# Performance work log

Hardware: AMD Instinct MI355X
Metric: run time of the kernel (lower is better)

Reference implementation:

```python
import jax, jax.numpy as jnp
import numpy as np

B, L, D, K, MAXL = 2, 1024, 256, 64, 1024
EPS = 1e-5

def _encode(x, pos, w1, b1, w2, b2, wa, ba):
    # x: [B,L,D] -> complex phasors [B,L,K]
    xa = x + pos[: x.shape[1]][None]
    h = jax.nn.gelu(xa @ w1 + b1, approximate=False)
    phase = jnp.tanh(h @ w2 + b2) * np.float32(np.pi)
    amp = jax.nn.softplus(xa @ wa + ba) + np.float32(0.1)
    return (amp * jnp.exp(1j * phase)).astype(jnp.complex64)

def setup_inputs() -> dict:
    key = jax.random.key(0)
    ks = jax.random.split(key, 24)
    def lin_w(k, i, o):
        return (jax.random.normal(k, (i, o), jnp.float32) / np.sqrt(np.float32(i)))
    def pos(k):
        return jax.random.normal(k, (MAXL, D), jnp.float32) * np.float32(0.02)
    inp = {
        'x': jax.random.normal(ks[0], (B, L, D), jnp.float32),
        'pos_k': pos(ks[1]),
        'w1_k': lin_w(ks[2], D, D), 'b1_k': jnp.zeros((D,), jnp.float32),
        'w2_k': lin_w(ks[3], D, K), 'b2_k': jnp.zeros((K,), jnp.float32),
        'wa_k': lin_w(ks[4], D, K), 'ba_k': jnp.zeros((K,), jnp.float32),
        'pos_q': pos(ks[5]),
        'w1_q': lin_w(ks[6], D, D), 'b1_q': jnp.zeros((D,), jnp.float32),
        'w2_q': lin_w(ks[7], D, K), 'b2_q': jnp.zeros((K,), jnp.float32),
        'wa_q': lin_w(ks[8], D, K), 'ba_q': jnp.zeros((K,), jnp.float32),
        'wv': lin_w(ks[9], D, D), 'bv': jnp.zeros((D,), jnp.float32),
        'ln_g': jnp.ones((D,), jnp.float32), 'ln_b': jnp.zeros((D,), jnp.float32),
        'wo': lin_w(ks[10], D, D), 'bo': jnp.zeros((D,), jnp.float32),
    }
    return inp

def reference(x, pos_k, w1_k, b1_k, w2_k, b2_k, wa_k, ba_k,
              pos_q, w1_q, b1_q, w2_q, b2_q, wa_q, ba_q,
              wv, bv, ln_g, ln_b, wo, bo):
    Bx, Lx, Dx = x.shape
    kp = _encode(x, pos_k, w1_k, b1_k, w2_k, b2_k, wa_k, ba_k)  # [B,L,K] complex
    qp = _encode(x, pos_q, w1_q, b1_q, w2_q, b2_q, wa_q, ba_q)  # [B,L,K] complex
    V = (x @ wv + bv).astype(jnp.complex64)                      # [B,L,D]
    bound = kp[:, :, :, None] * V[:, :, None, :]                 # [B,L,K,D]
    memory = jnp.cumsum(bound, axis=1)                           # [B,L,K,D]
    retrieved = jnp.real(jnp.einsum('blkd,blk->bld', memory, jnp.conj(qp)))
    positions = jnp.arange(1, Lx + 1, dtype=jnp.float32)
    norm = jnp.sqrt(positions * np.float32(kp.shape[-1]))[None, :, None]
    r = retrieved / norm
    mu = jnp.mean(r, axis=-1, keepdims=True)
    var = jnp.var(r, axis=-1, keepdims=True)
    rn = (r - mu) / jnp.sqrt(var + np.float32(EPS)) * ln_g + ln_b
    return x + rn @ wo + bo
```

## Files before the change

kernel.cpp:

```cpp
#include <hip/hip_runtime.h>
#include <hip/hip_bf16.h>

typedef __attribute__((ext_vector_type(8))) short short8;
typedef __attribute__((ext_vector_type(4))) float float4v;

constexpr int B = 2, L = 1024, D = 256, K = 64;
constexpr int N = B * L;
constexpr int NC = L / 64;

constexpr int WT2_OFF = 524288;

__device__ __forceinline__ ushort bf16_hi(float v) {
  return (ushort)(__float_as_uint(v) >> 16);
}
__device__ __forceinline__ float hi_f(float v) {
  return __uint_as_float(__float_as_uint(v) & 0xFFFF0000u);
}
__device__ __forceinline__ ushort bf16_rne(float v) {
  uint b = __float_as_uint(v);
  b += 0x7FFF + ((b >> 16) & 1);
  return (ushort)(b >> 16);
}

__global__ __launch_bounds__(256) void prep_kernel(
    const float* __restrict__ w1_k, const float* __restrict__ w1_q,
    const float* __restrict__ wv, const float* __restrict__ wo,
    const float* __restrict__ w2_k, const float* __restrict__ wa_k,
    const float* __restrict__ w2_q, const float* __restrict__ wa_q,
    ushort* __restrict__ WT) {
  __shared__ float Lt[64][65];
  const int bi = blockIdx.x, tid = threadIdx.x;
  const float* src;
  int ncols, k0, n0;
  ushort* dhi;
  int losz;
  if (bi < 64) {
    const int m = bi >> 4, t = bi & 15;
    src = (m == 0) ? w1_k : (m == 1) ? w1_q : (m == 2) ? wv : wo;
    ncols = 256; k0 = (t >> 2) * 64; n0 = (t & 3) * 64;
    dhi = WT + m * 131072; losz = 65536;
  } else {
    const int m = (bi - 64) >> 2, kt = (bi - 64) & 3;
    src = (m == 0) ? w2_k : (m == 1) ? wa_k : (m == 2) ? w2_q : wa_q;
    ncols = 64; k0 = kt * 64; n0 = 0;
    dhi = WT + WT2_OFF + m * 32768; losz = 16384;
  }
  ushort* dlo = dhi + losz;
  for (int p = 0; p < 16; ++p) {
    const int kr = p * 4 + (tid >> 6), nc = tid & 63;
    Lt[kr][nc] = src[(k0 + kr) * ncols + n0 + nc];
  }
  __syncthreads();
  const int n = tid >> 2, kq = tid & 3;
  uint uh[8], ul[8];
  for (int i = 0; i < 8; ++i) {
    const float v0 = Lt[kq * 16 + 2 * i][n];
    const float v1 = Lt[kq * 16 + 2 * i + 1][n];
    uh[i] = (uint)bf16_hi(v0) | ((uint)bf16_hi(v1) << 16);
    ul[i] = (uint)bf16_rne(v0 - hi_f(v0)) | ((uint)bf16_rne(v1 - hi_f(v1)) << 16);
  }
  const int oidx = (n0 + n) * 256 + k0 + kq * 16;
  *(uint4*)&dhi[oidx] = make_uint4(uh[0], uh[1], uh[2], uh[3]);
  *(uint4*)&dhi[oidx + 8] = make_uint4(uh[4], uh[5], uh[6], uh[7]);
  *(uint4*)&dlo[oidx] = make_uint4(ul[0], ul[1], ul[2], ul[3]);
  *(uint4*)&dlo[oidx + 8] = make_uint4(ul[4], ul[5], ul[6], ul[7]);
}

__global__ __launch_bounds__(256) void enc1_kernel(
    const float* __restrict__ x, const float* __restrict__ pos_k,
    const float* __restrict__ pos_q,
    const float* __restrict__ b1_k, const float* __restrict__ b1_q,
    const float* __restrict__ bv, const ushort* __restrict__ WT,
    float* __restrict__ hk, float* __restrict__ hq, float* __restrict__ V) {
  __shared__ __align__(16) ushort Ah[32][40], Al[32][40];
  __shared__ __align__(16) ushort Bh[128][40], Bl[128][40];
  const int tid = threadIdx.x;
  const int g = blockIdx.x / 128;
  const int rem = blockIdx.x % 128;
  const int row0 = (rem >> 1) * 32, nb = (rem & 1) * 128;
  const float* pos = (g == 0) ? pos_k : (g == 1) ? pos_q : nullptr;
  const ushort* Wh = WT + g * 131072;
  const ushort* Wl = Wh + 65536;
  const int w = tid >> 6, lane = tid & 63;
  const int m16 = lane & 15, quad = lane >> 4;

  float4v acc[2][2] = {};

  for (int k0 = 0; k0 < 256; k0 += 32) {
    __syncthreads();
    {
      const int r = tid >> 3, kc = (tid & 7) * 4;
      const int row = row0 + r, l = row & (L - 1);
      float4 xv = *(const float4*)&x[row * D + k0 + kc];
      if (pos) {
        const float4 pv = *(const float4*)&pos[l * D + k0 + kc];
        xv.x += pv.x; xv.y += pv.y; xv.z += pv.z; xv.w += pv.w;
      }
      ushort4 h4, l4;
      h4.x = bf16_hi(xv.x); l4.x = bf16_rne(xv.x - hi_f(xv.x));
      h4.y = bf16_hi(xv.y); l4.y = bf16_rne(xv.y - hi_f(xv.y));
      h4.z = bf16_hi(xv.z); l4.z = bf16_rne(xv.z - hi_f(xv.z));
      h4.w = bf16_hi(xv.w); l4.w = bf16_rne(xv.w - hi_f(xv.w));
      *(ushort4*)&Ah[r][kc] = h4;
      *(ushort4*)&Al[r][kc] = l4;
    }
#pragma unroll
    for (int p = 0; p < 2; ++p) {
      const int n = (tid >> 2) + p * 64, chunk = tid & 3;
      const int ga = (nb + n) * 256 + k0 + chunk * 8;
      *(uint4*)&Bh[n][chunk * 8] = *(const uint4*)&Wh[ga];
      *(uint4*)&Bl[n][chunk * 8] = *(const uint4*)&Wl[ga];
    }
    __syncthreads();

    short8 afh[2], afl[2], bfh[2], bfl[2];
#pragma unroll
    for (int r = 0; r < 2; ++r) {
      afh[r] = *(const short8*)&Ah[r * 16 + m16][quad * 8];
      afl[r] = *(const short8*)&Al[r * 16 + m16][quad * 8];
    }
#pragma unroll
    for (int c = 0; c < 2; ++c) {
      const int col = w * 32 + c * 16 + m16;
      bfh[c] = *(const short8*)&Bh[col][quad * 8];
      bfl[c] = *(const short8*)&Bl[col][quad * 8];
    }
#pragma unroll
    for (int r = 0; r < 2; ++r)
#pragma unroll
      for (int c = 0; c < 2; ++c) {
        acc[r][c] = __builtin_amdgcn_mfma_f32_16x16x32_bf16(afh[r], bfh[c], acc[r][c], 0, 0, 0);
        acc[r][c] = __builtin_amdgcn_mfma_f32_16x16x32_bf16(afh[r], bfl[c], acc[r][c], 0, 0, 0);
        acc[r][c] = __builtin_amdgcn_mfma_f32_16x16x32_bf16(afl[r], bfh[c], acc[r][c], 0, 0, 0);
      }
  }

  float* outp = (g == 0) ? hk : (g == 1) ? hq : V;
  const float* bp = (g == 0) ? b1_k : (g == 1) ? b1_q : bv;
#pragma unroll
  for (int c = 0; c < 2; ++c) {
    const int colg = nb + w * 32 + c * 16 + m16;
    const float bias = bp[colg];
#pragma unroll
    for (int r = 0; r < 2; ++r)
#pragma unroll
      for (int j = 0; j < 4; ++j) {
        const int rowg = row0 + r * 16 + quad * 4 + j;
        float v = acc[r][c][j] + bias;
        if (g < 2) v = 0.5f * v * (1.0f + erff(v * 0.70710678f));
        outp[rowg * D + colg] = v;
      }
  }
}

__global__ __launch_bounds__(512) void enc2_kernel(
    const float* __restrict__ x, const float* __restrict__ pos_k,
    const float* __restrict__ pos_q, const float* __restrict__ hk,
    const float* __restrict__ hq,
    const float* __restrict__ b2_k, const float* __restrict__ ba_k,
    const float* __restrict__ b2_q, const float* __restrict__ ba_q,
    const ushort* __restrict__ WT,
    float* __restrict__ kr, float* __restrict__ ki,
    float* __restrict__ qr, float* __restrict__ qi) {
  __shared__ __align__(16) ushort Ahh[16][40], Ahl[16][40], Axh[16][40], Axl[16][40];
  __shared__ __align__(16) ushort B2h[64][40], B2l[64][40], Bah[64][40], Bal[64][40];
  __shared__ float phL[16][68], amL[16][68];
  const int tid = threadIdx.x;
  const int e = blockIdx.x >> 7;
  const int r0g = (blockIdx.x & 127) * 16;
  const float* hsrc = e ? hq : hk;
  const float* pos = e ? pos_q : pos_k;
  const ushort* W2h = WT + WT2_OFF + (e ? 2 : 0) * 32768;
  const ushort* W2l = W2h + 16384;
  const ushort* Wah = WT + WT2_OFF + (e ? 3 : 1) * 32768;
  const ushort* Wal = Wah + 16384;
  const int w = tid >> 6, lane = tid & 63;
  const int m16 = lane & 15, quad = lane >> 4;
  const int mat = w & 1, ct = w >> 1;

  float4v acc = {};
  for (int k0 = 0; k0 < 256; k0 += 32) {
    __syncthreads();
    {
      const int half = tid >> 8;
      const int t2 = tid & 255;
      const int r = t2 >> 4, kc = (t2 & 15) * 2;
      const int row = r0g + r, l = row & (L - 1);
      if (half == 0) {
        const float2 hv = *(const float2*)&hsrc[row * D + k0 + kc];
        ushort2 h2, l2;
        h2.x = bf16_hi(hv.x); l2.x = bf16_rne(hv.x - hi_f(hv.x));
        h2.y = bf16_hi(hv.y); l2.y = bf16_rne(hv.y - hi_f(hv.y));
        *(ushort2*)&Ahh[r][kc] = h2;
        *(ushort2*)&Ahl[r][kc] = l2;
      } else {
        const float2 xv = *(const float2*)&x[row * D + k0 + kc];
        const float2 pv = *(const float2*)&pos[l * D + k0 + kc];
        const float a0 = xv.x + pv.x, a1 = xv.y + pv.y;
        ushort2 h2, l2;
        h2.x = bf16_hi(a0); l2.x = bf16_rne(a0 - hi_f(a0));
        h2.y = bf16_hi(a1); l2.y = bf16_rne(a1 - hi_f(a1));
        *(ushort2*)&Axh[r][kc] = h2;
        *(ushort2*)&Axl[r][kc] = l2;
      }
    }
    {
      const int sel = tid >> 7;
      const int idx = tid & 127;
      const int n = idx >> 1, ch = (idx & 1) * 2;
      const int ga = n * 256 + k0 + ch * 8;
      const ushort* s = (sel == 0) ? W2h : (sel == 1) ? W2l : (sel == 2) ? Wah : Wal;
      ushort* dst = (sel == 0) ? &B2h[n][ch * 8] : (sel == 1) ? &B2l[n][ch * 8]
                  : (sel == 2) ? &Bah[n][ch * 8] : &Bal[n][ch * 8];
      *(uint4*)dst = *(const uint4*)&s[ga];
      *(uint4*)(dst + 8) = *(const uint4*)&s[ga + 8];
    }
    __syncthreads();

    const short8 ah = mat ? *(const short8*)&Axh[m16][quad * 8]
                          : *(const short8*)&Ahh[m16][quad * 8];
    const short8 al = mat ? *(const short8*)&Axl[m16][quad * 8]
                          : *(const short8*)&Ahl[m16][quad * 8];
    const int col = ct * 16 + m16;
    const short8 bh = mat ? *(const short8*)&Bah[col][quad * 8]
                          : *(const short8*)&B2h[col][quad * 8];
    const short8 bl = mat ? *(const short8*)&Bal[col][quad * 8]
                          : *(const short8*)&B2l[col][quad * 8];
    acc = __builtin_amdgcn_mfma_f32_16x16x32_bf16(ah, bh, acc, 0, 0, 0);
    acc = __builtin_amdgcn_mfma_f32_16x16x32_bf16(ah, bl, acc, 0, 0, 0);
    acc = __builtin_amdgcn_mfma_f32_16x16x32_bf16(al, bh, acc, 0, 0, 0);
  }

  {
    const int colk = ct * 16 + m16;
    if (mat == 0) {
      const float b2v = (e ? b2_q : b2_k)[colk];
#pragma unroll
      for (int j = 0; j < 4; ++j)
        phL[quad * 4 + j][colk] = tanhf(acc[j] + b2v) * 3.14159265358979f;
    } else {
      const float bav = (e ? ba_q : ba_k)[colk];
#pragma unroll
      for (int j = 0; j < 4; ++j) {
        const float av = acc[j] + bav;
        amL[quad * 4 + j][colk] = fmaxf(av, 0.0f) + log1pf(expf(-fabsf(av))) + 0.1f;
      }
    }
  }
  __syncthreads();
  {
    float* pr = e ? qr : kr;
    float* pim = e ? qi : ki;
#pragma unroll
    for (int p = 0; p < 2; ++p) {
      const int idx = p * 512 + tid;
      const int r = idx >> 6, ccol = idx & 63;
      const int row = r0g + r;
      const float a = amL[r][ccol], pph = phL[r][ccol];
      pr[row * K + ccol] = a * cosf(pph);
      pim[row * K + ccol] = a * sinf(pph);
    }
  }
}

__global__ __launch_bounds__(256) void tbuild_kernel(
    const float* __restrict__ kr, const float* __restrict__ ki,
    const float* __restrict__ V, float* __restrict__ TMt) {
  const int id = blockIdx.x;
  const int dc = id & 15, c = (id >> 4) & 15, b = id >> 8;
  const int tid = threadIdx.x;
  const int n0 = b * L + c * 64;
  const int dl = tid & 15;
  const int kb = tid >> 4;

  __shared__ float krL[64][68], kiL[64][68];
  __shared__ float VL[64][20];
  __shared__ float Tl[16][204];
  for (int e = tid; e < 1024; e += 256) {
    const int t = e >> 4, k4 = (e & 15) * 4;
    *(float4*)&krL[t][k4] = *(const float4*)&kr[(n0 + t) * K + k4];
    *(float4*)&kiL[t][k4] = *(const float4*)&ki[(n0 + t) * K + k4];
  }
  {
    const int t = tid >> 2, f = (tid & 3) * 4;
    *(float4*)&VL[t][f] = *(const float4*)&V[(n0 + t) * D + dc * 16 + f];
  }
  __syncthreads();

  {
    const int t0 = (tid >> 4) * 4;
#pragma unroll
    for (int i = 0; i < 4; ++i) Tl[dl][128 + t0 + i] = VL[t0 + i][dl];
  }

  float ar[4] = {0.f, 0.f, 0.f, 0.f}, ai[4] = {0.f, 0.f, 0.f, 0.f};
#pragma unroll 4
  for (int t = 0; t < 64; ++t) {
    const float vt = VL[t][dl];
    const float4 k4r = *(const float4*)&krL[t][kb * 4];
    const float4 k4i = *(const float4*)&kiL[t][kb * 4];
    ar[0] += k4r.x * vt; ar[1] += k4r.y * vt; ar[2] += k4r.z * vt; ar[3] += k4r.w * vt;
    ai[0] += k4i.x * vt; ai[1] += k4i.y * vt; ai[2] += k4i.z * vt; ai[3] += k4i.w * vt;
  }

#pragma unroll
  for (int i = 0; i < 4; ++i) {
    Tl[dl][kb * 4 + i] = ar[i];
    Tl[dl][64 + kb * 4 + i] = ai[i];
  }
  __syncthreads();

  float* dst = &TMt[(((size_t)(b * 16 + c)) * 256 + dc * 16) * 192];
#pragma unroll
  for (int p = 0; p < 3; ++p) {
    const int e = p * 256 + tid;
    const int row = e / 48, f4 = e % 48;
    *(float4*)&dst[(size_t)row * 192 + f4 * 4] = *(const float4*)&Tl[row][f4 * 4];
  }
}

__global__ __launch_bounds__(512) void ret_kernel(
    const float* __restrict__ qr, const float* __restrict__ qi,
    const float* __restrict__ kr, const float* __restrict__ ki,
    const float* __restrict__ TMt, float* __restrict__ ret,
    float* __restrict__ LNred) {
  __shared__ __align__(16) ushort Ah[64][200], Al[64][200];
  __shared__ __align__(16) ushort Kh[64][136], Kl[64][136];
  __shared__ __align__(16) ushort Bh[32][200], Bl[32][200];
  const int tid = threadIdx.x;
  const int dc = blockIdx.x & 7;
  const int c = (blockIdx.x >> 3) & 15;
  const int b = blockIdx.x >> 7;
  const int n0 = b * L + c * 64;
  const int cols0 = dc * 32;
  const int w = tid >> 6, lane = tid & 63;
  const int m16 = lane & 15, quad = lane >> 4;

#pragma unroll
  for (int j = 0; j < 4; ++j) {
    const int e = j * 512 + tid;
    const int row = e >> 5, c4 = e & 31;
    const int col0 = (c4 & 15) * 4;
    const int acol = (c4 < 16 ? 0 : 64) + col0;
    {
      const float* src = (c4 < 16) ? qr : qi;
      const float4 v = *(const float4*)&src[(n0 + row) * K + col0];
      ushort4 h4, l4;
      h4.x = bf16_hi(v.x); l4.x = bf16_rne(v.x - hi_f(v.x));
      h4.y = bf16_hi(v.y); l4.y = bf16_rne(v.y - hi_f(v.y));
      h4.z = bf16_hi(v.z); l4.z = bf16_rne(v.z - hi_f(v.z));
      h4.w = bf16_hi(v.w); l4.w = bf16_rne(v.w - hi_f(v.w));
      *(ushort4*)&Ah[row][acol] = h4;
      *(ushort4*)&Al[row][acol] = l4;
    }
    {
      const float* src = (c4 < 16) ? kr : ki;
      const float4 v = *(const float4*)&src[(n0 + row) * K + col0];
      ushort4 h4, l4;
      h4.x = bf16_hi(v.x); l4.x = bf16_rne(v.x - hi_f(v.x));
      h4.y = bf16_hi(v.y); l4.y = bf16_rne(v.y - hi_f(v.y));
      h4.z = bf16_hi(v.z); l4.z = bf16_rne(v.z - hi_f(v.z));
      h4.w = bf16_hi(v.w); l4.w = bf16_rne(v.w - hi_f(v.w));
      *(ushort4*)&Kh[row][acol] = h4;
      *(ushort4*)&Kl[row][acol] = l4;
    }
  }

  float4 mac0 = {}, mac1 = {};
  {
    const int prow = tid >> 4, in0 = (tid & 15) * 8;
    const float* base = &TMt[(size_t)(b * 16) * 256 * 192 +
                             (size_t)(cols0 + prow) * 192 + in0];
    for (int cp = 0; cp < c; ++cp) {
      const float* p = base + (size_t)cp * 256 * 192;
      const float4 v0 = *(const float4*)p;
      const float4 v1 = *(const float4*)(p + 4);
      mac0.x += v0.x; mac0.y += v0.y; mac0.z += v0.z; mac0.w += v0.w;
      mac1.x += v1.x; mac1.y += v1.y; mac1.z += v1.z; mac1.w += v1.w;
    }
  }
  __syncthreads();

  {
    const int rt = w & 3;
    const int cp = (w >> 2) * 2;
    float4v sc[2] = {};
#pragma unroll
    for (int kk = 0; kk < 128; kk += 32) {
      const short8 ah = *(const short8*)&Ah[rt * 16 + m16][kk + quad * 8];
      const short8 al = *(const short8*)&Al[rt * 16 + m16][kk + quad * 8];
#pragma unroll
      for (int cc = 0; cc < 2; ++cc) {
        const int ct = cp + cc;
        const short8 bh = *(const short8*)&Kh[ct * 16 + m16][kk + quad * 8];
        const short8 bl = *(const short8*)&Kl[ct * 16 + m16][kk + quad * 8];
        sc[cc] = __builtin_amdgcn_mfma_f32_16x16x32_bf16(ah, bh, sc[cc], 0, 0, 0);
        sc[cc] = __builtin_amdgcn_mfma_f32_16x16x32_bf16(ah, bl, sc[cc], 0, 0, 0);
        sc[cc] = __builtin_amdgcn_mfma_f32_16x16x32_bf16(al, bh, sc[cc], 0, 0, 0);
      }
    }
#pragma unroll
    for (int cc = 0; cc < 2; ++cc)
#pragma unroll
      for (int j = 0; j < 4; ++j) {
        const int row = rt * 16 + quad * 4 + j;
        const int t = (cp + cc) * 16 + m16;
        const float s = (t <= row) ? sc[cc][j] : 0.0f;
        Ah[row][128 + t] = bf16_hi(s);
        Al[row][128 + t] = bf16_rne(s - hi_f(s));
      }
  }

  {
    const int prow = tid >> 4, in0 = (tid & 15) * 8;
    ushort4 h4, l4;
    h4.x = bf16_hi(mac0.x); l4.x = bf16_rne(mac0.x - hi_f(mac0.x));
    h4.y = bf16_hi(mac0.y); l4.y = bf16_rne(mac0.y - hi_f(mac0.y));
    h4.z = bf16_hi(mac0.z); l4.z = bf16_rne(mac0.z - hi_f(mac0.z));
    h4.w = bf16_hi(mac0.w); l4.w = bf16_rne(mac0.w - hi_f(mac0.w));
    *(ushort4*)&Bh[prow][in0] = h4;
    *(ushort4*)&Bl[prow][in0] = l4;
    h4.x = bf16_hi(mac1.x); l4.x = bf16_rne(mac1.x - hi_f(mac1.x));
    h4.y = bf16_hi(mac1.y); l4.y = bf16_rne(mac1.y - hi_f(mac1.y));
    h4.z = bf16_hi(mac1.z); l4.z = bf16_rne(mac1.z - hi_f(mac1.z));
    h4.w = bf16_hi(mac1.w); l4.w = bf16_rne(mac1.w - hi_f(mac1.w));
    *(ushort4*)&Bh[prow][in0 + 4] = h4;
    *(ushort4*)&Bl[prow][in0 + 4] = l4;

    const int vrow = tid >> 4, vin = 128 + (tid & 15) * 4;
    const float4 v = *(const float4*)&TMt[(size_t)(b * 16 + c) * 256 * 192 +
                                          (size_t)(cols0 + vrow) * 192 + vin];
    ushort4 vh, vl;
    vh.x = bf16_hi(v.x); vl.x = bf16_rne(v.x - hi_f(v.x));
    vh.y = bf16_hi(v.y); vl.y = bf16_rne(v.y - hi_f(v.y));
    vh.z = bf16_hi(v.z); vl.z = bf16_rne(v.z - hi_f(v.z));
    vh.w = bf16_hi(v.w); vl.w = bf16_rne(v.w - hi_f(v.w));
    *(ushort4*)&Bh[vrow][vin] = vh;
    *(ushort4*)&Bl[vrow][vin] = vl;
  }
  __syncthreads();

  {
    const int rt = w & 3;
    const int ct = w >> 2;
    float4v r2 = {};
#pragma unroll
    for (int kk = 0; kk < 6; ++kk) {
      const short8 ah = *(const short8*)&Ah[rt * 16 + m16][kk * 32 + quad * 8];
      const short8 al = *(const short8*)&Al[rt * 16 + m16][kk * 32 + quad * 8];
      const short8 bh = *(const short8*)&Bh[ct * 16 + m16][kk * 32 + quad * 8];
      const short8 bl = *(const short8*)&Bl[ct * 16 + m16][kk * 32 + quad * 8];
      r2 = __builtin_amdgcn_mfma_f32_16x16x32_bf16(ah, bh, r2, 0, 0, 0);
      r2 = __builtin_amdgcn_mfma_f32_16x16x32_bf16(ah, bl, r2, 0, 0, 0);
      r2 = __builtin_amdgcn_mfma_f32_16x16x32_bf16(al, bh, r2, 0, 0, 0);
    }
#pragma unroll
    for (int j = 0; j < 4; ++j) {
      const int rowL = rt * 16 + quad * 4 + j;
      const float nrm = rsqrtf((float)(c * 64 + rowL + 1) * 64.0f);
      const float v = r2[j] * nrm;
      ret[(size_t)(n0 + rowL) * D + cols0 + ct * 16 + m16] = v;
      float sj = v, s2j = v * v;
      for (int off = 1; off < 16; off <<= 1) {
        sj += __shfl_xor(sj, off, 64);
        s2j += __shfl_xor(s2j, off, 64);
      }
      if (m16 == 0) {
        LNred[(size_t)(n0 + rowL) * 32 + (dc * 2 + ct) * 2 + 0] = sj;
        LNred[(size_t)(n0 + rowL) * 32 + (dc * 2 + ct) * 2 + 1] = s2j;
      }
    }
  }
}

__global__ __launch_bounds__(512) void out2_kernel(
    const float* __restrict__ ret, const float* __restrict__ LNred,
    const float* __restrict__ x, const float* __restrict__ ln_g,
    const float* __restrict__ ln_b, const ushort* __restrict__ WT,
    const float* __restrict__ bo, float* __restrict__ out) {
  __shared__ __align__(16) ushort Ah[32][40], Al[32][40];
  __shared__ __align__(16) ushort Bh[64][40], Bl[64][40];
  __shared__ float mu_s[32], rs_s[32];
  const int tid = threadIdx.x;
  const int row0 = (blockIdx.x >> 2) * 32, nb = (blockIdx.x & 3) * 64;
  const ushort* Wh = WT + 3 * 131072;
  const ushort* Wl = Wh + 65536;
  const int w = tid >> 6, lane = tid & 63;
  const int m16 = lane & 15, quad = lane >> 4;
  const int rt = w & 1, cq = w >> 1;

  if (tid < 32) {
    const int row = row0 + tid;
    float s = 0.f, s2 = 0.f;
#pragma unroll
    for (int i = 0; i < 16; ++i) {
      s += LNred[(size_t)row * 32 + i * 2 + 0];
      s2 += LNred[(size_t)row * 32 + i * 2 + 1];
    }
    const float mu = s * (1.0f / 256.0f);
    mu_s[tid] = mu;
    rs_s[tid] = rsqrtf(s2 * (1.0f / 256.0f) - mu * mu + 1e-5f);
  }

  float4v acc = {};
  for (int k0 = 0; k0 < 256; k0 += 32) {
    __syncthreads();
    {
      const int r = tid >> 4, kc = (tid & 15) * 2;
      const float2 v = *(const float2*)&ret[(size_t)(row0 + r) * D + k0 + kc];
      const float2 g2 = *(const float2*)&ln_g[k0 + kc];
      const float2 b2 = *(const float2*)&ln_b[k0 + kc];
      const float mu = mu_s[r], rs = rs_s[r];
      const float a0 = (v.x - mu) * rs * g2.x + b2.x;
      const float a1 = (v.y - mu) * rs * g2.y + b2.y;
      ushort2 h2, l2;
      h2.x = bf16_hi(a0); l2.x = bf16_rne(a0 - hi_f(a0));
      h2.y = bf16_hi(a1); l2.y = bf16_rne(a1 - hi_f(a1));
      *(ushort2*)&Ah[r][kc] = h2;
      *(ushort2*)&Al[r][kc] = l2;
    }
    {
      const int plane = tid >> 8;
      const int n = (tid >> 2) & 63, chunk = tid & 3;
      const int ga = (nb + n) * 256 + k0 + chunk * 8;
      if (plane == 0) *(uint4*)&Bh[n][chunk * 8] = *(const uint4*)&Wh[ga];
      else            *(uint4*)&Bl[n][chunk * 8] = *(const uint4*)&Wl[ga];
    }
    __syncthreads();

    const short8 afh = *(const short8*)&Ah[rt * 16 + m16][quad * 8];
    const short8 afl = *(const short8*)&Al[rt * 16 + m16][quad * 8];
    const int col = cq * 16 + m16;
    const short8 bfh = *(const short8*)&Bh[col][quad * 8];
    const short8 bfl = *(const short8*)&Bl[col][quad * 8];
    acc = __builtin_amdgcn_mfma_f32_16x16x32_bf16(afh, bfh, acc, 0, 0, 0);
    acc = __builtin_amdgcn_mfma_f32_16x16x32_bf16(afh, bfl, acc, 0, 0, 0);
    acc = __builtin_amdgcn_mfma_f32_16x16x32_bf16(afl, bfh, acc, 0, 0, 0);
  }

  const int colg = nb + cq * 16 + m16;
  const float bias = bo[colg];
#pragma unroll
  for (int j = 0; j < 4; ++j) {
    const int rowg = row0 + rt * 16 + quad * 4 + j;
    out[rowg * D + colg] = x[rowg * D + colg] + acc[j] + bias;
  }
}

extern "C" void kernel_launch(void* const* d_in, const int* in_sizes, int n_in,
                              void* d_out, int out_size, void* d_ws, size_t ws_size,
                              hipStream_t stream) {
  (void)in_sizes; (void)n_in; (void)out_size; (void)ws_size;
  const float* x    = (const float*)d_in[0];
  const float* pos_k= (const float*)d_in[1];
  const float* w1_k = (const float*)d_in[2];
  const float* b1_k = (const float*)d_in[3];
  const float* w2_k = (const float*)d_in[4];
  const float* b2_k = (const float*)d_in[5];
  const float* wa_k = (const float*)d_in[6];
  const float* ba_k = (const float*)d_in[7];
  const float* pos_q= (const float*)d_in[8];
  const float* w1_q = (const float*)d_in[9];
  const float* b1_q = (const float*)d_in[10];
  const float* w2_q = (const float*)d_in[11];
  const float* b2_q = (const float*)d_in[12];
  const float* wa_q = (const float*)d_in[13];
  const float* ba_q = (const float*)d_in[14];
  const float* wv   = (const float*)d_in[15];
  const float* bv   = (const float*)d_in[16];
  const float* ln_g = (const float*)d_in[17];
  const float* ln_b = (const float*)d_in[18];
  const float* wo   = (const float*)d_in[19];
  const float* bo   = (const float*)d_in[20];

  float* ws = (float*)d_ws;
  float* kr = ws;
  float* ki = kr + (size_t)N * K;
  float* qr = ki + (size_t)N * K;
  float* qi = qr + (size_t)N * K;
  float* V  = qi + (size_t)N * K;
  float* TMt = V + (size_t)N * D;
  float* ret = TMt + (size_t)B * NC * 256 * 192;
  float* LNred = ret + (size_t)N * D;
  float* hk = LNred + (size_t)N * 32;
  float* hq = hk + (size_t)N * D;
  ushort* WT = (ushort*)(hq + (size_t)N * D);

  prep_kernel<<<80, 256, 0, stream>>>(w1_k, w1_q, wv, wo,
                                      w2_k, wa_k, w2_q, wa_q, WT);
  enc1_kernel<<<384, 256, 0, stream>>>(x, pos_k, pos_q, b1_k, b1_q, bv, WT,
                                       hk, hq, V);
  enc2_kernel<<<256, 512, 0, stream>>>(x, pos_k, pos_q, hk, hq,
                                       b2_k, ba_k, b2_q, ba_q, WT,
                                       kr, ki, qr, qi);
  tbuild_kernel<<<B * NC * 16, 256, 0, stream>>>(kr, ki, V, TMt);
  ret_kernel<<<B * NC * 8, 512, 0, stream>>>(qr, qi, kr, ki, TMt, ret, LNred);
  out2_kernel<<<256, 512, 0, stream>>>(ret, LNred, x, ln_g, ln_b, WT, bo,
                                       (float*)d_out);
}
```

Before: 148.4 us.

## Load MFMA operands directly from global in retrieval; halve enc1 column tile

The retrieval kernel stops staging Q, K and the running memory prefix in large shared buffers. Each lane now loads its own MFMA fragments from global memory and converts them to split bf16 in registers, keeping only the masked score tile in shared memory. This cuts LDS footprint and one barrier, at the cost of redundant global loads. Separately, enc1 uses a 64-column tile with twice as many blocks to raise parallelism and occupancy.

Measured after the change: 173.4 us. 16.8% more time.

```diff
diff --git a/kernel.cpp b/kernel.cpp
--- a/kernel.cpp
+++ b/kernel.cpp
@@ -20,6 +20,15 @@
   uint b = __float_as_uint(v);
   b += 0x7FFF + ((b >> 16) & 1);
   return (ushort)(b >> 16);
+}
+__device__ __forceinline__ void cvt8(const float4 a, const float4 b,
+                                     short8& h, short8& l) {
+  const float v[8] = {a.x, a.y, a.z, a.w, b.x, b.y, b.z, b.w};
+#pragma unroll
+  for (int i = 0; i < 8; ++i) {
+    h[i] = (short)bf16_hi(v[i]);
+    l[i] = (short)bf16_rne(v[i] - hi_f(v[i]));
+  }
 }
 
 __global__ __launch_bounds__(256) void prep_kernel(
@@ -73,18 +82,18 @@
     const float* __restrict__ bv, const ushort* __restrict__ WT,
     float* __restrict__ hk, float* __restrict__ hq, float* __restrict__ V) {
   __shared__ __align__(16) ushort Ah[32][40], Al[32][40];
-  __shared__ __align__(16) ushort Bh[128][40], Bl[128][40];
+  __shared__ __align__(16) ushort Bh[64][40], Bl[64][40];
   const int tid = threadIdx.x;
-  const int g = blockIdx.x / 128;
-  const int rem = blockIdx.x % 128;
-  const int row0 = (rem >> 1) * 32, nb = (rem & 1) * 128;
+  const int g = blockIdx.x / 256;
+  const int rem = blockIdx.x % 256;
+  const int row0 = (rem >> 2) * 32, nb = (rem & 3) * 64;
   const float* pos = (g == 0) ? pos_k : (g == 1) ? pos_q : nullptr;
   const ushort* Wh = WT + g * 131072;
   const ushort* Wl = Wh + 65536;
   const int w = tid >> 6, lane = tid & 63;
   const int m16 = lane & 15, quad = lane >> 4;
 
-  float4v acc[2][2] = {};
+  float4v acc[2] = {};
 
   for (int k0 = 0; k0 < 256; k0 += 32) {
     __syncthreads();
@@ -104,53 +113,44 @@
       *(ushort4*)&Ah[r][kc] = h4;
       *(ushort4*)&Al[r][kc] = l4;
     }
-#pragma unroll
-    for (int p = 0; p < 2; ++p) {
-      const int n = (tid >> 2) + p * 64, chunk = tid & 3;
+    {
+      const int n = tid >> 2, chunk = tid & 3;
       const int ga = (nb + n) * 256 + k0 + chunk * 8;
       *(uint4*)&Bh[n][chunk * 8] = *(const uint4*)&Wh[ga];
       *(uint4*)&Bl[n][chunk * 8] = *(const uint4*)&Wl[ga];
     }
     __syncthreads();
 
-    short8 afh[2], afl[2], bfh[2], bfl[2];
+    short8 afh[2], afl[2];
 #pragma unroll
     for (int r = 0; r < 2; ++r) {
       afh[r] = *(const short8*)&Ah[r * 16 + m16][quad * 8];
       afl[r] = *(const short8*)&Al[r * 16 + m16][quad * 8];
     }
-#pragma unroll
-    for (int c = 0; c < 2; ++c) {
-      const int col = w * 32 + c * 16 + m16;
-      bfh[c] = *(const short8*)&Bh[col][quad * 8];
-      bfl[c] = *(const short8*)&Bl[col][quad * 8];
-    }
-#pragma unroll
-    for (int r = 0; r < 2; ++r)
-#pragma unroll
-      for (int c = 0; c < 2; ++c) {
-        acc[r][c] = __builtin_amdgcn_mfma_f32_16x16x32_bf16(afh[r], bfh[c], acc[r][c], 0, 0, 0);
-        acc[r][c] = __builtin_amdgcn_mfma_f32_16x16x32_bf16(afh[r], bfl[c], acc[r][c], 0, 0, 0);
-        acc[r][c] = __builtin_amdgcn_mfma_f32_16x16x32_bf16(afl[r], bfh[c], acc[r][c], 0, 0, 0);
-      }
+    const int col = w * 16 + m16;
+    const short8 bfh = *(const short8*)&Bh[col][quad * 8];
+    const short8 bfl = *(const short8*)&Bl[col][quad * 8];
+#pragma unroll
+    for (int r = 0; r < 2; ++r) {
+      acc[r] = __builtin_amdgcn_mfma_f32_16x16x32_bf16(afh[r], bfh, acc[r], 0, 0, 0);
+      acc[r] = __builtin_amdgcn_mfma_f32_16x16x32_bf16(afh[r], bfl, acc[r], 0, 0, 0);
+      acc[r] = __builtin_amdgcn_mfma_f32_16x16x32_bf16(afl[r], bfh, acc[r], 0, 0, 0);
+    }
   }
 
   float* outp = (g == 0) ? hk : (g == 1) ? hq : V;
   const float* bp = (g == 0) ? b1_k : (g == 1) ? b1_q : bv;
-#pragma unroll
-  for (int c = 0; c < 2; ++c) {
-    const int colg = nb + w * 32 + c * 16 + m16;
-    const float bias = bp[colg];
-#pragma unroll
-    for (int r = 0; r < 2; ++r)
-#pragma unroll
-      for (int j = 0; j < 4; ++j) {
-        const int rowg = row0 + r * 16 + quad * 4 + j;
-        float v = acc[r][c][j] + bias;
-        if (g < 2) v = 0.5f * v * (1.0f + erff(v * 0.70710678f));
-        outp[rowg * D + colg] = v;
-      }
-  }
+  const int colg = nb + w * 16 + m16;
+  const float bias = bp[colg];
+#pragma unroll
+  for (int r = 0; r < 2; ++r)
+#pragma unroll
+    for (int j = 0; j < 4; ++j) {
+      const int rowg = row0 + r * 16 + quad * 4 + j;
+      float v = acc[r][j] + bias;
+      if (g < 2) v = 0.5f * v * (1.0f + erff(v * 0.70710678f));
+      outp[rowg * D + colg] = v;
+    }
 }
 
 __global__ __launch_bounds__(512) void enc2_kernel(
@@ -324,9 +324,7 @@
     const float* __restrict__ kr, const float* __restrict__ ki,
     const float* __restrict__ TMt, float* __restrict__ ret,
     float* __restrict__ LNred) {
-  __shared__ __align__(16) ushort Ah[64][200], Al[64][200];
-  __shared__ __align__(16) ushort Kh[64][136], Kl[64][136];
-  __shared__ __align__(16) ushort Bh[32][200], Bl[32][200];
+  __shared__ __align__(16) ushort Sh[64][72], Sl[64][72];
   const int tid = threadIdx.x;
   const int dc = blockIdx.x & 7;
   const int c = (blockIdx.x >> 3) & 15;
@@ -335,130 +333,101 @@
   const int cols0 = dc * 32;
   const int w = tid >> 6, lane = tid & 63;
   const int m16 = lane & 15, quad = lane >> 4;
-
-#pragma unroll
-  for (int j = 0; j < 4; ++j) {
-    const int e = j * 512 + tid;
-    const int row = e >> 5, c4 = e & 31;
-    const int col0 = (c4 & 15) * 4;
-    const int acol = (c4 < 16 ? 0 : 64) + col0;
-    {
-      const float* src = (c4 < 16) ? qr : qi;
-      const float4 v = *(const float4*)&src[(n0 + row) * K + col0];
-      ushort4 h4, l4;
-      h4.x = bf16_hi(v.x); l4.x = bf16_rne(v.x - hi_f(v.x));
-      h4.y = bf16_hi(v.y); l4.y = bf16_rne(v.y - hi_f(v.y));
-      h4.z = bf16_hi(v.z); l4.z = bf16_rne(v.z - hi_f(v.z));
-      h4.w = bf16_hi(v.w); l4.w = bf16_rne(v.w - hi_f(v.w));
-      *(ushort4*)&Ah[row][acol] = h4;
-      *(ushort4*)&Al[row][acol] = l4;
-    }
-    {
-      const float* src = (c4 < 16) ? kr : ki;
-      const float4 v = *(const float4*)&src[(n0 + row) * K + col0];
-      ushort4 h4, l4;
-      h4.x = bf16_hi(v.x); l4.x = bf16_rne(v.x - hi_f(v.x));
-      h4.y = bf16_hi(v.y); l4.y = bf16_rne(v.y - hi_f(v.y));
-      h4.z = bf16_hi(v.z); l4.z = bf16_rne(v.z - hi_f(v.z));
-      h4.w = bf16_hi(v.w); l4.w = bf16_rne(v.w - hi_f(v.w));
-      *(ushort4*)&Kh[row][acol] = h4;
-      *(ushort4*)&Kl[row][acol] = l4;
-    }
-  }
-
-  float4 mac0 = {}, mac1 = {};
-  {
-    const int prow = tid >> 4, in0 = (tid & 15) * 8;
-    const float* base = &TMt[(size_t)(b * 16) * 256 * 192 +
-                             (size_t)(cols0 + prow) * 192 + in0];
+  const int rt = w & 3, ct = w >> 2;
+
+  float m[4][8] = {};
+  {
+    const int n = cols0 + ct * 16 + m16;
+    const float* base = TMt + (size_t)(b * 16) * 49152 + (size_t)n * 192 + quad * 8;
     for (int cp = 0; cp < c; ++cp) {
-      const float* p = base + (size_t)cp * 256 * 192;
-      const float4 v0 = *(const float4*)p;
-      const float4 v1 = *(const float4*)(p + 4);
-      mac0.x += v0.x; mac0.y += v0.y; mac0.z += v0.z; mac0.w += v0.w;
-      mac1.x += v1.x; mac1.y += v1.y; mac1.z += v1.z; mac1.w += v1.w;
-    }
-  }
-  __syncthreads();
-
-  {
-    const int rt = w & 3;
-    const int cp = (w >> 2) * 2;
+      const float* p = base + (size_t)cp * 49152;
+#pragma unroll
+      for (int s = 0; s < 4; ++s) {
+        const float4 v0 = *(const float4*)(p + s * 32);
+        const float4 v1 = *(const float4*)(p + s * 32 + 4);
+        m[s][0] += v0.x; m[s][1] += v0.y; m[s][2] += v0.z; m[s][3] += v0.w;
+        m[s][4] += v1.x; m[s][5] += v1.y; m[s][6] += v1.z; m[s][7] += v1.w;
+      }
+    }
+  }
+
+  {
     float4v sc[2] = {};
 #pragma unroll
-    for (int kk = 0; kk < 128; kk += 32) {
-      const short8 ah = *(const short8*)&Ah[rt * 16 + m16][kk + quad * 8];
-      const short8 al = *(const short8*)&Al[rt * 16 + m16][kk + quad * 8];
-#pragma unroll
-      for (int cc = 0; cc < 2; ++cc) {
-        const int ct = cp + cc;
-        const short8 bh = *(const short8*)&Kh[ct * 16 + m16][kk + quad * 8];
-        const short8 bl = *(const short8*)&Kl[ct * 16 + m16][kk + quad * 8];
-        sc[cc] = __builtin_amdgcn_mfma_f32_16x16x32_bf16(ah, bh, sc[cc], 0, 0, 0);
-        sc[cc] = __builtin_amdgcn_mfma_f32_16x16x32_bf16(ah, bl, sc[cc], 0, 0, 0);
-        sc[cc] = __builtin_amdgcn_mfma_f32_16x16x32_bf16(al, bh, sc[cc], 0, 0, 0);
-      }
-    }
-#pragma unroll
-    for (int cc = 0; cc < 2; ++cc)
+    for (int kk = 0; kk < 4; ++kk) {
+      const float* qsrc = (kk < 2) ? qr : qi;
+      const int qoff = (kk & 1) * 32 + quad * 8;
+      const float4 qa = *(const float4*)&qsrc[(n0 + rt * 16 + m16) * K + qoff];
+      const float4 qb = *(const float4*)&qsrc[(n0 + rt * 16 + m16) * K + qoff + 4];
+      short8 ah, al;
+      cvt8(qa, qb, ah, al);
+#pragma unroll
+      for (int cf = 0; cf < 2; ++cf) {
+        const int t = ct * 32 + cf * 16 + m16;
+        const float* ksrc = (kk < 2) ? kr : ki;
+        const float4 ka = *(const float4*)&ksrc[(n0 + t) * K + qoff];
+        const float4 kb2 = *(const float4*)&ksrc[(n0 + t) * K + qoff + 4];
+        short8 bh, bl;
+        cvt8(ka, kb2, bh, bl);
+        sc[cf] = __builtin_amdgcn_mfma_f32_16x16x32_bf16(ah, bh, sc[cf], 0, 0, 0);
+        sc[cf] = __builtin_amdgcn_mfma_f32_16x16x32_bf16(ah, bl, sc[cf], 0, 0, 0);
+        sc[cf] = __builtin_amdgcn_mfma_f32_16x16x32_bf16(al, bh, sc[cf], 0, 0, 0);
+      }
+    }
+#pragma unroll
+    for (int cf = 0; cf < 2; ++cf)
 #pragma unroll
       for (int j = 0; j < 4; ++j) {
         const int row = rt * 16 + quad * 4 + j;
-        const int t = (cp + cc) * 16 + m16;
-        const float s = (t <= row) ? sc[cc][j] : 0.0f;
-        Ah[row][128 + t] = bf16_hi(s);
-        Al[row][128 + t] = bf16_rne(s - hi_f(s));
-      }
-  }
-
-  {
-    const int prow = tid >> 4, in0 = (tid & 15) * 8;
-    ushort4 h4, l4;
-    h4.x = bf16_hi(mac0.x); l4.x = bf16_rne(mac0.x - hi_f(mac0.x));
-    h4.y = bf16_hi(mac0.y); l4.y = bf16_rne(mac0.y - hi_f(mac0.y));
-    h4.z = bf16_hi(mac0.z); l4.z = bf16_rne(mac0.z - hi_f(mac0.z));
-    h4.w = bf16_hi(mac0.w); l4.w = bf16_rne(mac0.w - hi_f(mac0.w));
-    *(ushort4*)&Bh[prow][in0] = h4;
-    *(ushort4*)&Bl[prow][in0] = l4;
-    h4.x = bf16_hi(mac1.x); l4.x = bf16_rne(mac1.x - hi_f(mac1.x));
-    h4.y = bf16_hi(mac1.y); l4.y = bf16_rne(mac1.y - hi_f(mac1.y));
-    h4.z = bf16_hi(mac1.z); l4.z = bf16_rne(mac1.z - hi_f(mac1.z));
-    h4.w = bf16_hi(mac1.w); l4.w = bf16_rne(mac1.w - hi_f(mac1.w));
-    *(ushort4*)&Bh[prow][in0 + 4] = h4;
-    *(ushort4*)&Bl[prow][in0 + 4] = l4;
-
-    const int vrow = tid >> 4, vin = 128 + (tid & 15) * 4;
-    const float4 v = *(const float4*)&TMt[(size_t)(b * 16 + c) * 256 * 192 +
-                                          (size_t)(cols0 + vrow) * 192 + vin];
-    ushort4 vh, vl;
-    vh.x = bf16_hi(v.x); vl.x = bf16_rne(v.x - hi_f(v.x));
-    vh.y = bf16_hi(v.y); vl.y = bf16_rne(v.y - hi_f(v.y));
-    vh.z = bf16_hi(v.z); vl.z = bf16_rne(v.z - hi_f(v.z));
-    vh.w = bf16_hi(v.w); vl.w = bf16_rne(v.w - hi_f(v.w));
-    *(ushort4*)&Bh[vrow][vin] = vh;
-    *(ushort4*)&Bl[vrow][vin] = vl;
+        const int t = ct * 32 + cf * 16 + m16;
+        const float s = (t <= row) ? sc[cf][j] : 0.0f;
+        Sh[row][t] = bf16_hi(s);
+        Sl[row][t] = bf16_rne(s - hi_f(s));
+      }
   }
   __syncthreads();
 
   {
-    const int rt = w & 3;
-    const int ct = w >> 2;
-    float4v r2 = {};
-#pragma unroll
-    for (int kk = 0; kk < 6; ++kk) {
-      const short8 ah = *(const short8*)&Ah[rt * 16 + m16][kk * 32 + quad * 8];
-      const short8 al = *(const short8*)&Al[rt * 16 + m16][kk * 32 + quad * 8];
-      const short8 bh = *(const short8*)&Bh[ct * 16 + m16][kk * 32 + quad * 8];
-      const short8 bl = *(const short8*)&Bl[ct * 16 + m16][kk * 32 + quad * 8];
-      r2 = __builtin_amdgcn_mfma_f32_16x16x32_bf16(ah, bh, r2, 0, 0, 0);
-      r2 = __builtin_amdgcn_mfma_f32_16x16x32_bf16(ah, bl, r2, 0, 0, 0);
-      r2 = __builtin_amdgcn_mfma_f32_16x16x32_bf16(al, bh, r2, 0, 0, 0);
-    }
+    float4v racc = {};
+#pragma unroll
+    for (int s = 0; s < 4; ++s) {
+      const float* qsrc = (s < 2) ? qr : qi;
+      const int qoff = (s & 1) * 32 + quad * 8;
+      const float4 qa = *(const float4*)&qsrc[(n0 + rt * 16 + m16) * K + qoff];
+      const float4 qb = *(const float4*)&qsrc[(n0 + rt * 16 + m16) * K + qoff + 4];
+      short8 ah, al;
+      cvt8(qa, qb, ah, al);
+      short8 bh, bl;
+#pragma unroll
+      for (int i = 0; i < 8; ++i) {
+        bh[i] = (short)bf16_hi(m[s][i]);
+        bl[i] = (short)bf16_rne(m[s][i] - hi_f(m[s][i]));
+      }
+      racc = __builtin_amdgcn_mfma_f32_16x16x32_bf16(ah, bh, racc, 0, 0, 0);
+      racc = __builtin_amdgcn_mfma_f32_16x16x32_bf16(ah, bl, racc, 0, 0, 0);
+      racc = __builtin_amdgcn_mfma_f32_16x16x32_bf16(al, bh, racc, 0, 0, 0);
+    }
+#pragma unroll
+    for (int s2 = 0; s2 < 2; ++s2) {
+      const short8 ah = *(const short8*)&Sh[rt * 16 + m16][s2 * 32 + quad * 8];
+      const short8 al = *(const short8*)&Sl[rt * 16 + m16][s2 * 32 + quad * 8];
+      const int n = cols0 + ct * 16 + m16;
+      const float* vp = &TMt[(size_t)(b * 16 + c) * 49152 + (size_t)n * 192 +
+                             128 + s2 * 32 + quad * 8];
+      const float4 va = *(const float4*)vp;
+      const float4 vb = *(const float4*)(vp + 4);
+      short8 bh, bl;
+      cvt8(va, vb, bh, bl);
+      racc = __builtin_amdgcn_mfma_f32_16x16x32_bf16(ah, bh, racc, 0, 0, 0);
+      racc = __builtin_amdgcn_mfma_f32_16x16x32_bf16(ah, bl, racc, 0, 0, 0);
+      racc = __builtin_amdgcn_mfma_f32_16x16x32_bf16(al, bh, racc, 0, 0, 0);
+    }
+
 #pragma unroll
     for (int j = 0; j < 4; ++j) {
       const int rowL = rt * 16 + quad * 4 + j;
       const float nrm = rsqrtf((float)(c * 64 + rowL + 1) * 64.0f);
-      const float v = r2[j] * nrm;
+      const float v = racc[j] * nrm;
       ret[(size_t)(n0 + rowL) * D + cols0 + ct * 16 + m16] = v;
       float sj = v, s2j = v * v;
       for (int off = 1; off < 16; off <<= 1) {
@@ -588,7 +557,7 @@
 
   prep_kernel<<<80, 256, 0, stream>>>(w1_k, w1_q, wv, wo,
                                       w2_k, wa_k, w2_q, wa_q, WT);
-  enc1_kernel<<<384, 256, 0, stream>>>(x, pos_k, pos_q, b1_k, b1_q, bv, WT,
+  enc1_kernel<<<768, 256, 0, stream>>>(x, pos_k, pos_q, b1_k, b1_q, bv, WT,
                                        hk, hq, V);
   enc2_kernel<<<256, 512, 0, stream>>>(x, pos_k, pos_q, hk, hq,
                                        b2_k, ba_k, b2_q, ba_q, WT,
```
